# Kernel optimization log

Hardware: AMD Instinct MI355X
Metric: run time of the kernel (lower is better)

## Reference

```python
import jax, jax.numpy as jnp
import numpy as np

LEN_EPISODE = 1000
DT = 0.01
B = 65536


def setup_inputs() -> dict:
    key = jax.random.key(0)
    k1, k2 = jax.random.split(key)
    init_conds = jax.random.normal(k1, (B, 2), dtype=jnp.float32)
    # params columns: omega, gamma, A, phi (all positive -> friction & forcing active)
    params = jax.random.uniform(k2, (B, 4), dtype=jnp.float32)
    return {"init_conds": init_conds, "params": params}


def _dynamics(t, y, omega, gamma, A, phi):
    # y: [B, 2] = (theta, theta_dot); omega/gamma/A/phi: [B, 1]
    th = y[:, 0:1]
    thdot = y[:, 1:2]
    force = A * omega * omega * jnp.cos(2.0 * jnp.pi * phi * t)
    acc = force - gamma * thdot - omega * omega * jnp.sin(th)
    return jnp.concatenate([thdot, acc], axis=-1)


def _integrate(init_conds, params):
    omega = params[:, 0:1]
    gamma = params[:, 1:2]
    A = params[:, 2:3]
    phi = params[:, 3:4]
    dt = jnp.float32(DT)
    ts = jnp.linspace(0.0, DT * (LEN_EPISODE - 1), LEN_EPISODE, dtype=jnp.float32)

    def rk4_step(y, t):
        k1 = _dynamics(t, y, omega, gamma, A, phi)
        k2 = _dynamics(t + 0.5 * dt, y + 0.5 * dt * k1, omega, gamma, A, phi)
        k3 = _dynamics(t + 0.5 * dt, y + 0.5 * dt * k2, omega, gamma, A, phi)
        k4 = _dynamics(t + dt, y + dt * k3, omega, gamma, A, phi)
        y_next = y + (dt / 6.0) * (k1 + 2.0 * k2 + 2.0 * k3 + k4)
        return y_next, y_next[:, 0]

    _, thetas = jax.lax.scan(rk4_step, init_conds, ts[:-1])  # thetas: [T-1, B]
    x = jnp.concatenate([init_conds[:, 0][None, :], thetas], axis=0)  # [T, B]
    return x.T  # [B, T] (matches x[:, :, 0].permute(1, 0))


def reference(init_conds, params):
    return _integrate(init_conds, params)
```

## Files before the change

kernel.cpp:

```cpp
#include <hip/hip_runtime.h>


typedef float v2f __attribute__((ext_vector_type(2)));

__device__ __forceinline__ v2f vfma2(v2f a, v2f b, v2f c) {
#if __has_builtin(__builtin_elementwise_fma)
    return __builtin_elementwise_fma(a, b, c);
#else
    v2f r; r.x = fmaf(a.x, b.x, c.x); r.y = fmaf(a.y, b.y, c.y); return r;
#endif
}
__device__ __forceinline__ v2f splat2(float v) { v2f r; r.x = v; r.y = v; return r; }

#define CHI_F 0.15915494309189533577f
#define CLO_F ((float)(0.15915494309189533577 - (double)0.15915494309189533577f))
#define MAGIC_F 12582912.0f

__device__ __forceinline__ v2f to_rev2(v2f x) {
    v2f nb = vfma2(x, splat2(CHI_F), splat2(MAGIC_F));
    v2f n  = nb - splat2(MAGIC_F);
    v2f r  = vfma2(x, splat2(CHI_F), -n);
    r = vfma2(x, splat2(CLO_F), r);
    return r;
}
__device__ __forceinline__ float to_rev1(float x) {
    float nb = fmaf(x, CHI_F, MAGIC_F);
    float n  = nb - MAGIC_F;
    float r  = fmaf(x, CHI_F, -n);
    return fmaf(x, CLO_F, r);
}

__device__ __forceinline__ float hw_sin_rev(float x) {
#if __has_builtin(__builtin_amdgcn_sinf)
    return __builtin_amdgcn_sinf(x);
#else
    return __sinf(x * 6.28318530717958647692f);
#endif
}
__device__ __forceinline__ float hw_cos_rev(float x) {
#if __has_builtin(__builtin_amdgcn_cosf)
    return __builtin_amdgcn_cosf(x);
#else
    return __cosf(x * 6.28318530717958647692f);
#endif
}

__global__ __launch_bounds__(256) void pend_kernel(
    const float* __restrict__ init,
    const float* __restrict__ params,
    float* __restrict__ out,
    int B)
{
    int b = blockIdx.x * blockDim.x + threadIdx.x;
    if (b >= B) return;

    float th = init[2 * b + 0];
    float w  = init[2 * b + 1];
    const float omega = params[4 * b + 0];
    const float gamma = params[4 * b + 1];
    const float A     = params[4 * b + 2];
    const float phi   = params[4 * b + 3];

    const float dt  = 0.01f;
    const float hdt = 0.5f * dt;
    const float dt6 = dt / 6.0f;
    const float om2 = omega * omega;
    const float Fco = (A * omega) * omega;
    const float tp  = 6.28318530717958647692f * phi;

    float4* out4 = (float4*)(out + (size_t)b * 1000);

    float fk = 0.0f;

    auto step = [&]() -> float {
        float t  = fk * dt;
        fk += 1.0f;
        float t2 = t + hdt;
        float t3 = t + dt;
        v2f y12; y12.x = tp * t; y12.y = tp * t2;
        float y3  = tp * t3;
        float th2 = fmaf(hdt, w, th);

        v2f ra; ra.x = th; ra.y = th2;
        v2f rA = to_rev2(ra);
        v2f rB = to_rev2(y12);
        float r3 = to_rev1(y3);

        float sth = hw_sin_rev(rA.x);
        float s2  = hw_sin_rev(rA.y);
        float c1  = hw_cos_rev(rB.x);
        float c2  = hw_cos_rev(rB.y);
        float c4  = hw_cos_rev(r3);

        float a1  = Fco * c1 - gamma * w   - om2 * sth;
        float w2_ = fmaf(hdt, a1, w);
        float a2  = Fco * c2 - gamma * w2_ - om2 * s2;
        float th3 = fmaf(hdt, w2_, th);
        float s3  = hw_sin_rev(to_rev1(th3));
        float w3_ = fmaf(hdt, a2, w);
        float a3  = Fco * c2 - gamma * w3_ - om2 * s3;
        float th4 = fmaf(dt, w3_, th);
        float s4  = hw_sin_rev(to_rev1(th4));
        float w4_ = fmaf(dt, a3, w);
        float a4  = Fco * c4 - gamma * w4_ - om2 * s4;

        float ks_th = w  + 2.0f * w2_ + 2.0f * w3_ + w4_;
        float ks_w  = a1 + 2.0f * a2  + 2.0f * a3  + a4;
        th = fmaf(dt6, ks_th, th);
        w  = fmaf(dt6, ks_w,  w);
        return th;
    };

    float4 ob;
    ob.x = th;
    ob.y = step();
    ob.z = step();
    ob.w = step();
    out4[0] = ob;

    for (int c = 1; c < 250; ++c) {
        ob.x = step();
        ob.y = step();
        ob.z = step();
        ob.w = step();
        out4[c] = ob;
    }
}

extern "C" void kernel_launch(void* const* d_in, const int* in_sizes, int n_in,
                              void* d_out, int out_size, void* d_ws, size_t ws_size,
                              hipStream_t stream) {
    const float* init   = (const float*)d_in[0];
    const float* params = (const float*)d_in[1];
    float* out = (float*)d_out;
    int B = in_sizes[0] / 2;

    int block = 256;
    int grid  = (B + block - 1) / block;
    hipLaunchKernelGGL(pend_kernel, dim3(grid), dim3(block), 0, stream,
                       init, params, out, B);
}
```

Measured before the change: 137.5 us.

## Split forcing-cosine computation into producer wavefront feeding solver via LDS

Each block now holds two wavefronts per 64 pendulums. One wavefront computes the time-dependent forcing cosines in chunks of 8 steps into a double-buffered shared array. The other wavefront, at raised priority, reads them and runs the serial RK4 recurrence and the output stores. The aim is to take the transcendental forcing work off the latency-bound critical path. In exchange it doubles the thread count per element, adds a block barrier every 8 steps, and adds LDS traffic.

```diff
diff --git a/kernel.cpp b/kernel.cpp
--- a/kernel.cpp
+++ b/kernel.cpp
@@ -45,85 +45,148 @@
 #endif
 }
 
-__global__ __launch_bounds__(256) void pend_kernel(
+#define CH 8
+#define NFULL 124
+
+__global__ __launch_bounds__(128) void pend_kernel(
     const float* __restrict__ init,
     const float* __restrict__ params,
     float* __restrict__ out,
     int B)
 {
-    int b = blockIdx.x * blockDim.x + threadIdx.x;
-    if (b >= B) return;
-
-    float th = init[2 * b + 0];
-    float w  = init[2 * b + 1];
-    const float omega = params[4 * b + 0];
-    const float gamma = params[4 * b + 1];
-    const float A     = params[4 * b + 2];
-    const float phi   = params[4 * b + 3];
+    __shared__ float4 fbuf[2][CH][64];
+
+    const int lane = threadIdx.x & 63;
+    const int wv   = threadIdx.x >> 6;
+    int b = blockIdx.x * 64 + lane;
+    const int bc = (b < B) ? b : (B - 1);
 
     const float dt  = 0.01f;
     const float hdt = 0.5f * dt;
     const float dt6 = dt / 6.0f;
-    const float om2 = omega * omega;
-    const float Fco = (A * omega) * omega;
-    const float tp  = 6.28318530717958647692f * phi;
-
-    float4* out4 = (float4*)(out + (size_t)b * 1000);
-
-    float fk = 0.0f;
-
-    auto step = [&]() -> float {
-        float t  = fk * dt;
-        fk += 1.0f;
-        float t2 = t + hdt;
-        float t3 = t + dt;
-        v2f y12; y12.x = tp * t; y12.y = tp * t2;
-        float y3  = tp * t3;
-        float th2 = fmaf(hdt, w, th);
-
-        v2f ra; ra.x = th; ra.y = th2;
-        v2f rA = to_rev2(ra);
-        v2f rB = to_rev2(y12);
-        float r3 = to_rev1(y3);
-
-        float sth = hw_sin_rev(rA.x);
-        float s2  = hw_sin_rev(rA.y);
-        float c1  = hw_cos_rev(rB.x);
-        float c2  = hw_cos_rev(rB.y);
-        float c4  = hw_cos_rev(r3);
-
-        float a1  = Fco * c1 - gamma * w   - om2 * sth;
-        float w2_ = fmaf(hdt, a1, w);
-        float a2  = Fco * c2 - gamma * w2_ - om2 * s2;
-        float th3 = fmaf(hdt, w2_, th);
-        float s3  = hw_sin_rev(to_rev1(th3));
-        float w3_ = fmaf(hdt, a2, w);
-        float a3  = Fco * c2 - gamma * w3_ - om2 * s3;
-        float th4 = fmaf(dt, w3_, th);
-        float s4  = hw_sin_rev(to_rev1(th4));
-        float w4_ = fmaf(dt, a3, w);
-        float a4  = Fco * c4 - gamma * w4_ - om2 * s4;
-
-        float ks_th = w  + 2.0f * w2_ + 2.0f * w3_ + w4_;
-        float ks_w  = a1 + 2.0f * a2  + 2.0f * a3  + a4;
-        th = fmaf(dt6, ks_th, th);
-        w  = fmaf(dt6, ks_w,  w);
-        return th;
-    };
-
-    float4 ob;
-    ob.x = th;
-    ob.y = step();
-    ob.z = step();
-    ob.w = step();
-    out4[0] = ob;
-
-    for (int c = 1; c < 250; ++c) {
-        ob.x = step();
-        ob.y = step();
-        ob.z = step();
-        ob.w = step();
-        out4[c] = ob;
+
+    if (wv == 1) {
+        const float phi = params[4 * bc + 3];
+        const float tp  = 6.28318530717958647692f * phi;
+        float fk = 0.0f;
+
+        auto produce = [&](int buf, int s) {
+            float t  = fk * dt;
+            float t2 = t + hdt;
+            float t3 = t + dt;
+            v2f y12; y12.x = tp * t; y12.y = tp * t2;
+            float y3 = tp * t3;
+            v2f rB   = to_rev2(y12);
+            float r3 = to_rev1(y3);
+            float4 f;
+            f.x = hw_cos_rev(rB.x);
+            f.y = hw_cos_rev(rB.y);
+            f.z = hw_cos_rev(r3);
+            f.w = 0.0f;
+            fbuf[buf][s][lane] = f;
+            fk += 1.0f;
+        };
+
+        #pragma unroll
+        for (int s = 0; s < CH; ++s) produce(0, s);
+        __syncthreads();
+
+        for (int j = 0; j < NFULL; ++j) {
+            int buf = (j + 1) & 1;
+            #pragma unroll
+            for (int s = 0; s < CH; ++s) produce(buf, s);
+            __syncthreads();
+        }
+    } else {
+        __builtin_amdgcn_s_setprio(1);
+
+        float th = init[2 * bc + 0];
+        float w  = init[2 * bc + 1];
+        const float omega = params[4 * bc + 0];
+        const float gamma = params[4 * bc + 1];
+        const float A     = params[4 * bc + 2];
+        const float om2 = omega * omega;
+        const float Fco = (A * omega) * omega;
+
+        float4* out4 = (float4*)(out + (size_t)bc * 1000);
+        const bool wr = (b < B);
+
+        auto step = [&](float4 f) -> float {
+            float th2 = fmaf(hdt, w, th);
+            v2f ra; ra.x = th; ra.y = th2;
+            v2f rA = to_rev2(ra);
+            float sth = hw_sin_rev(rA.x);
+            float s2  = hw_sin_rev(rA.y);
+
+            float a1  = Fco * f.x - gamma * w   - om2 * sth;
+            float w2_ = fmaf(hdt, a1, w);
+            float a2  = Fco * f.y - gamma * w2_ - om2 * s2;
+            float th3 = fmaf(hdt, w2_, th);
+            float s3  = hw_sin_rev(to_rev1(th3));
+            float w3_ = fmaf(hdt, a2, w);
+            float a3  = Fco * f.y - gamma * w3_ - om2 * s3;
+            float th4 = fmaf(dt, w3_, th);
+            float s4  = hw_sin_rev(to_rev1(th4));
+            float w4_ = fmaf(dt, a3, w);
+            float a4  = Fco * f.z - gamma * w4_ - om2 * s4;
+
+            float ks_th = w  + 2.0f * w2_ + 2.0f * w3_ + w4_;
+            float ks_w  = a1 + 2.0f * a2  + 2.0f * a3  + a4;
+            th = fmaf(dt6, ks_th, th);
+            w  = fmaf(dt6, ks_w,  w);
+            return th;
+        };
+
+        __syncthreads();
+
+        float4 ob;
+        ob.x = th;
+        int c = 0;
+
+        for (int j = 0; j < NFULL; ++j) {
+            const int buf = j & 1;
+            float4 f0 = fbuf[buf][0][lane];
+            float4 f1 = fbuf[buf][1][lane];
+            float4 f2 = fbuf[buf][2][lane];
+            float4 f3 = fbuf[buf][3][lane];
+            float4 f4 = fbuf[buf][4][lane];
+            float4 f5 = fbuf[buf][5][lane];
+            float4 f6 = fbuf[buf][6][lane];
+            float4 f7 = fbuf[buf][7][lane];
+
+            ob.y = step(f0);
+            ob.z = step(f1);
+            ob.w = step(f2);
+            if (wr) out4[c] = ob;
+            ob.x = step(f3);
+            ob.y = step(f4);
+            ob.z = step(f5);
+            ob.w = step(f6);
+            if (wr) out4[c + 1] = ob;
+            ob.x = step(f7);
+            c += 2;
+            __syncthreads();
+        }
+
+        {
+            float4 f0 = fbuf[0][0][lane];
+            float4 f1 = fbuf[0][1][lane];
+            float4 f2 = fbuf[0][2][lane];
+            float4 f3 = fbuf[0][3][lane];
+            float4 f4 = fbuf[0][4][lane];
+            float4 f5 = fbuf[0][5][lane];
+            float4 f6 = fbuf[0][6][lane];
+
+            ob.y = step(f0);
+            ob.z = step(f1);
+            ob.w = step(f2);
+            if (wr) out4[c] = ob;
+            ob.x = step(f3);
+            ob.y = step(f4);
+            ob.z = step(f5);
+            ob.w = step(f6);
+            if (wr) out4[c + 1] = ob;
+        }
     }
 }
 
@@ -135,8 +198,7 @@
     float* out = (float*)d_out;
     int B = in_sizes[0] / 2;
 
-    int block = 256;
-    int grid  = (B + block - 1) / block;
-    hipLaunchKernelGGL(pend_kernel, dim3(grid), dim3(block), 0, stream,
+    int nblocks = (B + 63) / 64;
+    hipLaunchKernelGGL(pend_kernel, dim3(nblocks), dim3(128), 0, stream,
                        init, params, out, B);
 }
```

After: 146.6 us. 1.07x slower.

## Batch forcing cosines ahead of RK4 steps and reuse range reductions

Applied to the files above, without the earlier changes.

Precomputes the time-only forcing cosines for eight steps at a time, off the serial state dependency chain, and batches their range reduction with packed float2 ops. The sin range reductions for the third and fourth RK4 stages now reuse the reduced theta from the first stage via a delta FMA instead of a full reduction. This shortens the latency-bound per-step chain and removes some ALU work. It uses more registers, and the delta-based reduction slightly changes rounding.

```diff
diff --git a/kernel.cpp b/kernel.cpp
--- a/kernel.cpp
+++ b/kernel.cpp
@@ -20,14 +20,7 @@
     v2f nb = vfma2(x, splat2(CHI_F), splat2(MAGIC_F));
     v2f n  = nb - splat2(MAGIC_F);
     v2f r  = vfma2(x, splat2(CHI_F), -n);
-    r = vfma2(x, splat2(CLO_F), r);
-    return r;
-}
-__device__ __forceinline__ float to_rev1(float x) {
-    float nb = fmaf(x, CHI_F, MAGIC_F);
-    float n  = nb - MAGIC_F;
-    float r  = fmaf(x, CHI_F, -n);
-    return fmaf(x, CLO_F, r);
+    return vfma2(x, splat2(CLO_F), r);
 }
 
 __device__ __forceinline__ float hw_sin_rev(float x) {
@@ -68,39 +61,47 @@
     const float Fco = (A * omega) * omega;
     const float tp  = 6.28318530717958647692f * phi;
 
+    v2f hd2; hd2.x = hdt; hd2.y = dt;
+
     float4* out4 = (float4*)(out + (size_t)b * 1000);
 
     float fk = 0.0f;
 
-    auto step = [&]() -> float {
-        float t  = fk * dt;
-        fk += 1.0f;
-        float t2 = t + hdt;
-        float t3 = t + dt;
-        v2f y12; y12.x = tp * t; y12.y = tp * t2;
-        float y3  = tp * t3;
+    auto forcing = [&](float fkv, float rvy1_in, float& c1o, float& c2o,
+                       float& c4o) {
+        float t   = fkv * dt;
+        v2f t23   = splat2(t) + hd2;
+        float y1  = tp * t;
+        v2f y23   = splat2(tp) * t23;
+        v2f dy    = y23 - splat2(y1);
+        v2f rvy   = vfma2(dy, splat2(CHI_F), splat2(rvy1_in));
+        c1o = hw_cos_rev(rvy1_in);
+        c2o = hw_cos_rev(rvy.x);
+        c4o = hw_cos_rev(rvy.y);
+    };
+    auto rvy1_pair = [&](float fkv) -> v2f {
+        v2f fkp; fkp.x = fkv; fkp.y = fkv + 1.0f;
+        v2f tpr = fkp * splat2(dt);
+        v2f y1p = splat2(tp) * tpr;
+        return to_rev2(y1p);
+    };
+
+    auto step = [&](float c1, float c2, float c4) -> float {
         float th2 = fmaf(hdt, w, th);
-
-        v2f ra; ra.x = th; ra.y = th2;
-        v2f rA = to_rev2(ra);
-        v2f rB = to_rev2(y12);
-        float r3 = to_rev1(y3);
-
-        float sth = hw_sin_rev(rA.x);
-        float s2  = hw_sin_rev(rA.y);
-        float c1  = hw_cos_rev(rB.x);
-        float c2  = hw_cos_rev(rB.y);
-        float c4  = hw_cos_rev(r3);
+        v2f pr; pr.x = th; pr.y = th2;
+        v2f rvp = to_rev2(pr);
+        float sth = hw_sin_rev(rvp.x);
+        float s2  = hw_sin_rev(rvp.y);
 
         float a1  = Fco * c1 - gamma * w   - om2 * sth;
         float w2_ = fmaf(hdt, a1, w);
         float a2  = Fco * c2 - gamma * w2_ - om2 * s2;
         float th3 = fmaf(hdt, w2_, th);
-        float s3  = hw_sin_rev(to_rev1(th3));
+        float s3  = hw_sin_rev(fmaf(th3 - th, CHI_F, rvp.x));
         float w3_ = fmaf(hdt, a2, w);
         float a3  = Fco * c2 - gamma * w3_ - om2 * s3;
         float th4 = fmaf(dt, w3_, th);
-        float s4  = hw_sin_rev(to_rev1(th4));
+        float s4  = hw_sin_rev(fmaf(th4 - th, CHI_F, rvp.x));
         float w4_ = fmaf(dt, a3, w);
         float a4  = Fco * c4 - gamma * w4_ - om2 * s4;
 
@@ -113,17 +114,51 @@
 
     float4 ob;
     ob.x = th;
-    ob.y = step();
-    ob.z = step();
-    ob.w = step();
-    out4[0] = ob;
+    {
+        v2f rp = rvy1_pair(0.0f);
+        float c1, c2, c4;
+        forcing(0.0f, rp.x, c1, c2, c4); ob.y = step(c1, c2, c4);
+        forcing(1.0f, rp.y, c1, c2, c4); ob.z = step(c1, c2, c4);
+        v2f rp2 = rvy1_pair(2.0f);
+        forcing(2.0f, rp2.x, c1, c2, c4); ob.w = step(c1, c2, c4);
+        out4[0] = ob;
+    }
+    fk = 3.0f;
 
-    for (int c = 1; c < 250; ++c) {
-        ob.x = step();
-        ob.y = step();
-        ob.z = step();
-        ob.w = step();
-        out4[c] = ob;
+    for (int j = 0; j < 124; ++j) {
+        float C1[8], C2[8], C4[8];
+        #pragma unroll
+        for (int s = 0; s < 8; s += 2) {
+            v2f rp = rvy1_pair(fk + (float)s);
+            forcing(fk + (float)s,        rp.x, C1[s],     C2[s],     C4[s]);
+            forcing(fk + (float)(s + 1),  rp.y, C1[s + 1], C2[s + 1], C4[s + 1]);
+        }
+        ob.x = step(C1[0], C2[0], C4[0]);
+        ob.y = step(C1[1], C2[1], C4[1]);
+        ob.z = step(C1[2], C2[2], C4[2]);
+        ob.w = step(C1[3], C2[3], C4[3]);
+        out4[2 * j + 1] = ob;
+        ob.x = step(C1[4], C2[4], C4[4]);
+        ob.y = step(C1[5], C2[5], C4[5]);
+        ob.z = step(C1[6], C2[6], C4[6]);
+        ob.w = step(C1[7], C2[7], C4[7]);
+        out4[2 * j + 2] = ob;
+        fk += 8.0f;
+    }
+
+    {
+        float C1[4], C2[4], C4[4];
+        v2f rp = rvy1_pair(fk);
+        forcing(fk,        rp.x, C1[0], C2[0], C4[0]);
+        forcing(fk + 1.0f, rp.y, C1[1], C2[1], C4[1]);
+        v2f rp2 = rvy1_pair(fk + 2.0f);
+        forcing(fk + 2.0f, rp2.x, C1[2], C2[2], C4[2]);
+        forcing(fk + 3.0f, rp2.y, C1[3], C2[3], C4[3]);
+        ob.x = step(C1[0], C2[0], C4[0]);
+        ob.y = step(C1[1], C2[1], C4[1]);
+        ob.z = step(C1[2], C2[2], C4[2]);
+        ob.w = step(C1[3], C2[3], C4[3]);
+        out4[249] = ob;
     }
 }
 
```

Measured after the change: 124.2 us. 9.6% less time.
